# Kernel optimization log

Hardware: AMD Instinct MI355X
Metric: run time of the kernel (lower is better)

The kernel has to match this reference:

```python
import jax, jax.numpy as jnp
import numpy as np

T, B, S = 32, 64, 128
V, WV, ENC, DEC, ATT = 50000, 512, 512, 512, 512
LAYERS, POOL = 2, 2
IN0 = WV + ENC  # input_feed concat


def _gru_cell(x, h, W_ih, b_ih, W_hh, b_hh):
    gi = x @ W_ih.T + b_ih
    gh = h @ W_hh.T + b_hh
    i_r, i_z, i_n = jnp.split(gi, 3, axis=-1)
    h_r, h_z, h_n = jnp.split(gh, 3, axis=-1)
    r = jax.nn.sigmoid(i_r + h_r)
    z = jax.nn.sigmoid(i_z + h_z)
    n = jnp.tanh(i_n + r * h_n)
    return (1.0 - z) * n + z * h


def setup_inputs() -> dict:
    key = jax.random.key(0)
    ks = iter(jax.random.split(key, 32))
    d = {}
    d['input'] = jax.random.randint(next(ks), (T, B), 0, V)
    d['hidden'] = jax.random.normal(next(ks), (LAYERS, B, DEC), jnp.float32)
    d['context'] = jax.random.normal(next(ks), (S, B, ENC), jnp.float32)
    d['src_pad_mask'] = jnp.zeros((B, S), jnp.float32)
    d['init_att'] = jax.random.normal(next(ks), (B, ENC), jnp.float32)
    sc = 0.05
    d['emb_W'] = jax.random.normal(next(ks), (V, WV), jnp.float32) * sc
    # stacked GRU params (layer0 input IN0, layer1 input DEC)
    d['W_ih0'] = jax.random.normal(next(ks), (3 * DEC, IN0), jnp.float32) * sc
    d['b_ih0'] = jnp.zeros((3 * DEC,), jnp.float32)
    d['W_hh0'] = jax.random.normal(next(ks), (3 * DEC, DEC), jnp.float32) * sc
    d['b_hh0'] = jnp.zeros((3 * DEC,), jnp.float32)
    d['W_ih1'] = jax.random.normal(next(ks), (3 * DEC, DEC), jnp.float32) * sc
    d['b_ih1'] = jnp.zeros((3 * DEC,), jnp.float32)
    d['W_hh1'] = jax.random.normal(next(ks), (3 * DEC, DEC), jnp.float32) * sc
    d['b_hh1'] = jnp.zeros((3 * DEC,), jnp.float32)
    # concat attention
    d['W_pre'] = jax.random.normal(next(ks), (ATT, ENC), jnp.float32) * sc
    d['b_pre'] = jnp.zeros((ATT,), jnp.float32)
    d['W_q'] = jax.random.normal(next(ks), (ATT, DEC), jnp.float32) * sc
    d['w_v'] = jax.random.normal(next(ks), (ATT,), jnp.float32) * sc
    # copy switch
    d['W_copy'] = jax.random.normal(next(ks), (1, ENC + DEC), jnp.float32) * sc
    d['b_copy'] = jnp.zeros((1,), jnp.float32)
    # readout
    d['W_read'] = jax.random.normal(next(ks), (DEC, WV + DEC + ENC), jnp.float32) * sc
    d['b_read'] = jnp.zeros((DEC,), jnp.float32)
    return d


def reference(input, hidden, context, src_pad_mask, init_att, emb_W,
              W_ih0, b_ih0, W_hh0, b_hh0, W_ih1, b_ih1, W_hh1, b_hh1,
              W_pre, b_pre, W_q, w_v, W_copy, b_copy, W_read, b_read):
    emb = emb_W[input]                     # [T,B,WV]
    ctx_bse = jnp.transpose(context, (1, 0, 2))  # [B,S,ENC]
    precompute = jnp.einsum('bse,ae->bsa', ctx_bse, W_pre) + b_pre  # [B,S,ATT]
    neg_inf = jnp.finfo(jnp.float32).min

    def step(carry, emb_t):
        h, cur_ctx = carry
        x = jnp.concatenate([emb_t, cur_ctx], axis=1)  # input_feed
        h0 = _gru_cell(x, h[0], W_ih0, b_ih0, W_hh0, b_hh0)
        out = _gru_cell(h0, h[1], W_ih1, b_ih1, W_hh1, b_hh1)
        h_new = jnp.stack([h0, out])
        # concat attention
        q = out @ W_q.T                                  # [B,ATT]
        energy = jnp.tanh(precompute + q[:, None, :]) @ w_v  # [B,S]
        energy = jnp.where(src_pad_mask > 0.5, neg_inf, energy)
        attn = jax.nn.softmax(energy, axis=-1)
        new_ctx = jnp.einsum('bs,bse->be', attn, ctx_bse)
        copy_prob = jax.nn.sigmoid(
            jnp.concatenate([out, new_ctx], axis=1) @ W_copy.T + b_copy)  # [B,1]
        readout = jnp.concatenate([emb_t, out, new_ctx], axis=1) @ W_read.T + b_read
        maxout = jnp.max(readout.reshape(B, DEC // POOL, POOL), axis=-1)  # [B,DEC/POOL]
        return (h_new, new_ctx), (maxout, attn, copy_prob)

    (hidden_f, cur_ctx_f), (g_outputs, c_outputs, copy_gates) = jax.lax.scan(
        step, (hidden, init_att), emb)
    attn_last = c_outputs[-1]
    return g_outputs, c_outputs, copy_gates, hidden_f, attn_last, cur_ctx_f
```

## Files before the change

kernel.cpp:

```cpp
#include <hip/hip_runtime.h>


#define OFF_EGI    0
#define OFF_EREAD  3145728
#define OFF_ATTPRE 4194304
#define OFF_Q      8388608
#define OFF_GI     8454144
#define OFF_GH     8847360
#define OFF_GI1    8847360
#define OFF_GH1    9240576
#define OFF_RO     9437184
#define OFF_H0     9568256
#define OFF_H1     9633792
#define OFF_CTX    9699328

#define OO_G    0
#define OO_C    524288
#define OO_CP   786432
#define OO_HID  788480
#define OO_AL   854016
#define OO_CTXF 862208

__device__ __forceinline__ float sigm(float x) {
    x = fminf(fmaxf(x, -30.f), 30.f);
    return 1.0f / (1.0f + __expf(-x));
}
__device__ __forceinline__ float tanh_(float x) {
    x = fminf(fmaxf(x, -15.f), 15.f);
    float e = __expf(-2.0f * x);
    return (1.0f - e) / (1.0f + e);
}
__device__ __forceinline__ float gru_out(float ir, float iz, float in_,
                                         float hr, float hz, float hn, float hp) {
    float r = sigm(ir + hr), z = sigm(iz + hz);
    float n = tanh_(in_ + r * hn);
    return (1.f - z) * n + z * hp;
}

__device__ __forceinline__ void gemm64(
    const float* __restrict__ xrow, const float* __restrict__ wrow,
    int kt0, int nkt, float* lds_x, float* lds_w,
    float* __restrict__ outp, int JW, int orow0, int j0,
    const float* __restrict__ addp, int addmode, int addJW)
{
    const int tid = threadIdx.x;
    const int tb4 = tid >> 4, tj4 = tid & 15;
    float acc[4][4];
#pragma unroll
    for (int a = 0; a < 4; ++a)
#pragma unroll
        for (int b = 0; b < 4; ++b) acc[a][b] = 0.f;

    for (int kt = kt0; kt < kt0 + nkt; ++kt) {
        const int kb = kt << 6;
        __syncthreads();
        {
            const int rl = tid >> 2;
#pragma unroll
            for (int i = 0; i < 4; ++i) {
                const int kk = ((tid & 3) << 4) + (i << 2);
                float4 xv = *(const float4*)(xrow + kb + kk);
                float4 wv = *(const float4*)(wrow + kb + kk);
                lds_x[(kk + 0) * 64 + rl] = xv.x;
                lds_x[(kk + 1) * 64 + rl] = xv.y;
                lds_x[(kk + 2) * 64 + rl] = xv.z;
                lds_x[(kk + 3) * 64 + rl] = xv.w;
                lds_w[(kk + 0) * 64 + rl] = wv.x;
                lds_w[(kk + 1) * 64 + rl] = wv.y;
                lds_w[(kk + 2) * 64 + rl] = wv.z;
                lds_w[(kk + 3) * 64 + rl] = wv.w;
            }
        }
        __syncthreads();
#pragma unroll 4
        for (int kk = 0; kk < 64; ++kk) {
            float4 xv = *(const float4*)(lds_x + kk * 64 + tb4 * 4);
            float4 wv = *(const float4*)(lds_w + kk * 64 + tj4 * 4);
            acc[0][0] += xv.x * wv.x; acc[0][1] += xv.x * wv.y;
            acc[0][2] += xv.x * wv.z; acc[0][3] += xv.x * wv.w;
            acc[1][0] += xv.y * wv.x; acc[1][1] += xv.y * wv.y;
            acc[1][2] += xv.y * wv.z; acc[1][3] += xv.y * wv.w;
            acc[2][0] += xv.z * wv.x; acc[2][1] += xv.z * wv.y;
            acc[2][2] += xv.z * wv.z; acc[2][3] += xv.z * wv.w;
            acc[3][0] += xv.w * wv.x; acc[3][1] += xv.w * wv.y;
            acc[3][2] += xv.w * wv.z; acc[3][3] += xv.w * wv.w;
        }
    }
#pragma unroll
    for (int ib = 0; ib < 4; ++ib) {
        const int row = tb4 * 4 + ib;
        const int jc = j0 + tj4 * 4;
        float4 r;
        r.x = acc[ib][0]; r.y = acc[ib][1]; r.z = acc[ib][2]; r.w = acc[ib][3];
        if (addmode == 1) {
            float4 bv = *(const float4*)(addp + jc);
            r.x += bv.x; r.y += bv.y; r.z += bv.z; r.w += bv.w;
        } else if (addmode == 2) {
            float4 bv = *(const float4*)(addp + (size_t)(orow0 + row) * addJW + jc);
            r.x += bv.x; r.y += bv.y; r.z += bv.z; r.w += bv.w;
        }
        *(float4*)(outp + (size_t)(orow0 + row) * JW + jc) = r;
    }
}

__global__ __launch_bounds__(256)
void k_upfront(const int* __restrict__ inp, const float* __restrict__ hid,
               const float* __restrict__ ctxin, const float* __restrict__ init_att,
               const float* __restrict__ embW,
               const float* __restrict__ W_ih0, const float* __restrict__ b_ih0,
               const float* __restrict__ W_read, const float* __restrict__ b_read,
               const float* __restrict__ W_pre, const float* __restrict__ b_pre,
               float* __restrict__ wsf)
{
    __shared__ float lds_x[4096], lds_w[4096];
    const int jid = blockIdx.x, tid = threadIdx.x, rl = tid >> 2;
    if (jid < 768) {
        const int mt = jid / 24, jt = jid % 24, j0 = jt << 6;
        const int idx = inp[mt * 64 + rl];
        gemm64(embW + (size_t)idx * 512, W_ih0 + (size_t)(j0 + rl) * 1024,
               0, 8, lds_x, lds_w, wsf + OFF_EGI, 1536, mt << 6, j0, b_ih0, 1, 0);
    } else if (jid < 1024) {
        const int r = jid - 768, mt = r >> 3, jt = r & 7, j0 = jt << 6;
        const int idx = inp[mt * 64 + rl];
        gemm64(embW + (size_t)idx * 512, W_read + (size_t)(j0 + rl) * 1536,
               0, 8, lds_x, lds_w, wsf + OFF_EREAD, 512, mt << 6, j0, b_read, 1, 0);
    } else if (jid < 2048) {
        const int r = jid - 1024, mt = r >> 3, jt = r & 7, j0 = jt << 6;
        const int m = (mt << 6) + rl, b = m >> 7, s = m & 127;
        gemm64(ctxin + (size_t)((s << 6) + b) * 512, W_pre + (size_t)(j0 + rl) * 512,
               0, 8, lds_x, lds_w, wsf + OFF_ATTPRE, 512, mt << 6, j0, b_pre, 1, 0);
    } else {
        const int job = jid - 2048, buf = job >> 1, half = job & 1;
        const float* src = buf == 0 ? hid : (buf == 1 ? hid + 32768 : init_att);
        float* dst = wsf + (buf == 0 ? OFF_H0 : (buf == 1 ? OFF_H1 : OFF_CTX)) + 32768;
        for (int i = 0; i < 64; ++i) {
            int e = half * 16384 + i * 256 + tid;
            dst[e] = src[e];
        }
    }
}

__global__ __launch_bounds__(256)
void k_gates(int t, const float* __restrict__ W_ih0,
             const float* __restrict__ W_hh0, const float* __restrict__ b_hh0,
             const float* __restrict__ W_hh1, const float* __restrict__ b_hh1,
             const float* __restrict__ W_read, float* __restrict__ wsf)
{
    __shared__ float lds_x[4096], lds_w[4096];
    const int blk = blockIdx.x, tid = threadIdx.x, rl = tid >> 2;
    const int prv = (t & 1) ^ 1;
    const float* ctx_prv = wsf + OFF_CTX + prv * 32768;
    const float* h0_prv  = wsf + OFF_H0 + prv * 32768;
    const float* h1_prv  = wsf + OFF_H1 + prv * 32768;
    if (blk < 96) {
        const int jt = blk >> 2, kq = blk & 3, j0 = jt << 6;
        gemm64(ctx_prv + rl * 512, W_ih0 + (size_t)(j0 + rl) * 1024 + 512,
               kq * 2, 2, lds_x, lds_w, wsf + OFF_GI + kq * 98304, 1536, 0, j0,
               wsf + OFF_EGI + (size_t)t * 98304, kq == 0 ? 2 : 0, 1536);
    } else if (blk < 192) {
        const int r = blk - 96, jt = r >> 2, kq = r & 3, j0 = jt << 6;
        gemm64(h0_prv + rl * 512, W_hh0 + (size_t)(j0 + rl) * 512,
               kq * 2, 2, lds_x, lds_w, wsf + OFF_GH + kq * 98304, 1536, 0, j0,
               b_hh0, kq == 0 ? 1 : 0, 0);
    } else if (blk < 240) {
        const int r = blk - 192, jt = r >> 1, kh = r & 1, j0 = jt << 6;
        gemm64(h1_prv + rl * 512, W_hh1 + (size_t)(j0 + rl) * 512,
               kh * 4, 4, lds_x, lds_w, wsf + OFF_GH1 + kh * 98304, 1536, 0, j0,
               b_hh1, kh == 0 ? 1 : 0, 0);
    } else {
        if (t == 0) return;
        const int r = blk - 240, mat = r >> 4, kh = (r >> 3) & 1, jt = r & 7, j0 = jt << 6;
        const float* X = mat ? ctx_prv : h1_prv;
        gemm64(X + rl * 512, W_read + (size_t)(j0 + rl) * 1536 + 512 + mat * 512,
               kh * 4, 4, lds_x, lds_w, wsf + OFF_RO + (mat * 2 + kh) * 32768, 512, 0, j0,
               nullptr, 0, 0);
    }
}

__global__ __launch_bounds__(256)
void k_h0(int t, float* __restrict__ wsf, float* __restrict__ dout)
{
    const int blk = blockIdx.x, tid = threadIdx.x;
    const int cur = t & 1, prv = cur ^ 1;
    if (blk < 16) {
        float* h0_cur = wsf + OFF_H0 + cur * 32768;
        const float* h0_prv = wsf + OFF_H0 + prv * 32768;
        const float* GIp = wsf + OFF_GI;
        const float* GHp = wsf + OFF_GH;
#pragma unroll
        for (int i = 0; i < 8; ++i) {
            const int e = (blk << 11) + (i << 8) + tid;
            const int b = e >> 9, c = e & 511;
            const int base = b * 1536 + c;
            float gr = 0, gz = 0, gn = 0, hr = 0, hz = 0, hn = 0;
#pragma unroll
            for (int p = 0; p < 4; ++p) {
                gr += GIp[p * 98304 + base];
                gz += GIp[p * 98304 + base + 512];
                gn += GIp[p * 98304 + base + 1024];
                hr += GHp[p * 98304 + base];
                hz += GHp[p * 98304 + base + 512];
                hn += GHp[p * 98304 + base + 1024];
            }
            float rr = sigm(gr + hr), zz = sigm(gz + hz);
            float nn = tanh_(gn + rr * hn);
            h0_cur[b * 512 + c] = (1.f - zz) * nn + zz * h0_prv[b * 512 + c];
        }
    } else {
        if (t == 0) return;
        const int r = blk - 16;
        const float* ERp = wsf + OFF_EREAD + (size_t)(t - 1) * 32768;
        const float* ROp = wsf + OFF_RO;
#pragma unroll
        for (int i = 0; i < 8; ++i) {
            const int e = (r << 11) + (i << 8) + tid;
            const int b = e >> 8, j2 = e & 255;
            const int bi = b * 512 + (j2 << 1);
            float v0 = ERp[bi] + ROp[bi] + ROp[32768 + bi] + ROp[65536 + bi] + ROp[98304 + bi];
            float v1 = ERp[bi + 1] + ROp[bi + 1] + ROp[32768 + bi + 1] + ROp[65536 + bi + 1] + ROp[98304 + bi + 1];
            dout[OO_G + (size_t)(t - 1) * 16384 + b * 256 + j2] = fmaxf(v0, v1);
        }
    }
}

__global__ __launch_bounds__(256)
void k_gi1(int t, const float* __restrict__ W_ih1, const float* __restrict__ b_ih1,
           float* __restrict__ wsf)
{
    __shared__ float lds_x[4096], lds_w[4096];
    const int blk = blockIdx.x, tid = threadIdx.x, rl = tid >> 2;
    const int cur = t & 1;
    const float* h0_cur = wsf + OFF_H0 + cur * 32768;
    const int jt = blk >> 2, kq = blk & 3, j0 = jt << 6;
    gemm64(h0_cur + rl * 512, W_ih1 + (size_t)(j0 + rl) * 512,
           kq * 2, 2, lds_x, lds_w, wsf + OFF_GI1 + kq * 98304, 1536, 0, j0,
           b_ih1, kq == 0 ? 1 : 0, 0);
}

__global__ __launch_bounds__(256)
void k_oq(int t, const float* __restrict__ W_q, float* __restrict__ wsf)
{
    __shared__ float s_o[64 * 129];
    __shared__ float s_w[64 * 64];
    const int blk = blockIdx.x, tid = threadIdx.x;
    const int cur = t & 1, prv = cur ^ 1;
    const float* GI1p = wsf + OFF_GI1;
    const float* GH1p = wsf + OFF_GH1;
    const float* h1_prv = wsf + OFF_H1 + prv * 32768;
    float* h1_cur = wsf + OFF_H1 + cur * 32768;
    const int jt = blk >> 2, kq = blk & 3, j0 = jt << 6;
    const int kbase = kq << 7;
    const int tb4 = tid >> 4, tj4 = tid & 15, rl = tid >> 2;

#pragma unroll
    for (int i = 0; i < 8; ++i) {
        const int f = (i << 8) + tid;
        const int b = f >> 5, c4 = f & 31;
        const int c = kbase + (c4 << 2);
        float4 ir = {0,0,0,0}, iz = ir, in4 = ir, hr = ir, hz = ir, hn = ir;
#pragma unroll
        for (int p = 0; p < 4; ++p) {
            const float* gp = GI1p + p * 98304 + b * 1536 + c;
            float4 a0 = *(const float4*)(gp);
            float4 a1 = *(const float4*)(gp + 512);
            float4 a2 = *(const float4*)(gp + 1024);
            ir.x += a0.x; ir.y += a0.y; ir.z += a0.z; ir.w += a0.w;
            iz.x += a1.x; iz.y += a1.y; iz.z += a1.z; iz.w += a1.w;
            in4.x += a2.x; in4.y += a2.y; in4.z += a2.z; in4.w += a2.w;
        }
#pragma unroll
        for (int p = 0; p < 2; ++p) {
            const float* gp = GH1p + p * 98304 + b * 1536 + c;
            float4 a0 = *(const float4*)(gp);
            float4 a1 = *(const float4*)(gp + 512);
            float4 a2 = *(const float4*)(gp + 1024);
            hr.x += a0.x; hr.y += a0.y; hr.z += a0.z; hr.w += a0.w;
            hz.x += a1.x; hz.y += a1.y; hz.z += a1.z; hz.w += a1.w;
            hn.x += a2.x; hn.y += a2.y; hn.z += a2.z; hn.w += a2.w;
        }
        float4 hp = *(const float4*)(h1_prv + b * 512 + c);
        float4 o;
        o.x = gru_out(ir.x, iz.x, in4.x, hr.x, hz.x, hn.x, hp.x);
        o.y = gru_out(ir.y, iz.y, in4.y, hr.y, hz.y, hn.y, hp.y);
        o.z = gru_out(ir.z, iz.z, in4.z, hr.z, hz.z, hn.z, hp.z);
        o.w = gru_out(ir.w, iz.w, in4.w, hr.w, hz.w, hn.w, hp.w);
        const int kl = c4 << 2;
        s_o[b * 129 + kl + 0] = o.x;
        s_o[b * 129 + kl + 1] = o.y;
        s_o[b * 129 + kl + 2] = o.z;
        s_o[b * 129 + kl + 3] = o.w;
        if (jt == 0) *(float4*)(h1_cur + b * 512 + c) = o;
    }

    float acc[4][4];
#pragma unroll
    for (int a = 0; a < 4; ++a)
#pragma unroll
        for (int b = 0; b < 4; ++b) acc[a][b] = 0.f;

    for (int kt = 0; kt < 2; ++kt) {
        __syncthreads();
        {
            const float* wrow = W_q + (size_t)(j0 + rl) * 512 + kbase + kt * 64;
#pragma unroll
            for (int i = 0; i < 4; ++i) {
                const int kk = ((tid & 3) << 4) + (i << 2);
                float4 wv = *(const float4*)(wrow + kk);
                s_w[(kk + 0) * 64 + rl] = wv.x;
                s_w[(kk + 1) * 64 + rl] = wv.y;
                s_w[(kk + 2) * 64 + rl] = wv.z;
                s_w[(kk + 3) * 64 + rl] = wv.w;
            }
        }
        __syncthreads();
#pragma unroll 4
        for (int kk = 0; kk < 64; ++kk) {
            const int ka = kt * 64 + kk;
            float x0 = s_o[(tb4 * 4 + 0) * 129 + ka];
            float x1 = s_o[(tb4 * 4 + 1) * 129 + ka];
            float x2 = s_o[(tb4 * 4 + 2) * 129 + ka];
            float x3 = s_o[(tb4 * 4 + 3) * 129 + ka];
            float4 wv = *(const float4*)(s_w + kk * 64 + tj4 * 4);
            acc[0][0] += x0 * wv.x; acc[0][1] += x0 * wv.y; acc[0][2] += x0 * wv.z; acc[0][3] += x0 * wv.w;
            acc[1][0] += x1 * wv.x; acc[1][1] += x1 * wv.y; acc[1][2] += x1 * wv.z; acc[1][3] += x1 * wv.w;
            acc[2][0] += x2 * wv.x; acc[2][1] += x2 * wv.y; acc[2][2] += x2 * wv.z; acc[2][3] += x2 * wv.w;
            acc[3][0] += x3 * wv.x; acc[3][1] += x3 * wv.y; acc[3][2] += x3 * wv.z; acc[3][3] += x3 * wv.w;
        }
    }
    float* Qp = wsf + OFF_Q + kq * 32768;
#pragma unroll
    for (int ib = 0; ib < 4; ++ib) {
        float4 r;
        r.x = acc[ib][0]; r.y = acc[ib][1]; r.z = acc[ib][2]; r.w = acc[ib][3];
        *(float4*)(Qp + (size_t)(tb4 * 4 + ib) * 512 + j0 + tj4 * 4) = r;
    }
}

__global__ __launch_bounds__(256)
void k_att(int t, const float* __restrict__ ctxin, const float* __restrict__ maskp,
           const float* __restrict__ w_v, const float* __restrict__ W_copy,
           const float* __restrict__ b_copy, float* __restrict__ wsf,
           float* __restrict__ dout)
{
    __shared__ float s_q[512];
    __shared__ float s_e[128];
    __shared__ float s_at[128];
    __shared__ float s_ctx[512];
    __shared__ float s_red[256];
    const int b = blockIdx.x, tid = threadIdx.x;
    const int cur = t & 1;
    float* ctx_cur = wsf + OFF_CTX + cur * 32768;
    const float* h1_cur = wsf + OFF_H1 + cur * 32768;
    const float* Qp = wsf + OFF_Q;
#pragma unroll
    for (int h = 0; h < 2; ++h) {
        const int a = h * 256 + tid;
        s_q[a] = Qp[b * 512 + a] + Qp[32768 + b * 512 + a]
               + Qp[65536 + b * 512 + a] + Qp[98304 + b * 512 + a];
    }
    __syncthreads();
    {
        const int wid = tid >> 6, lane = tid & 63;
        for (int s = wid; s < 128; s += 4) {
            const float* pre = wsf + OFF_ATTPRE + ((size_t)b * 128 + s) * 512;
            float acc = 0.f;
#pragma unroll
            for (int i = 0; i < 8; ++i) {
                const int a = lane + (i << 6);
                acc += tanh_(pre[a] + s_q[a]) * w_v[a];
            }
#pragma unroll
            for (int d2 = 1; d2 < 64; d2 <<= 1) acc += __shfl_xor(acc, d2, 64);
            if (lane == 0)
                s_e[s] = (maskp[b * 128 + s] > 0.5f) ? -3.0e38f : acc;
        }
    }
    __syncthreads();
    if (tid < 64) {
        float e0 = s_e[tid], e1 = s_e[tid + 64];
        float mx = fmaxf(e0, e1);
#pragma unroll
        for (int d2 = 1; d2 < 64; d2 <<= 1) mx = fmaxf(mx, __shfl_xor(mx, d2, 64));
        float x0 = __expf(e0 - mx), x1 = __expf(e1 - mx);
        float sm = x0 + x1;
#pragma unroll
        for (int d2 = 1; d2 < 64; d2 <<= 1) sm += __shfl_xor(sm, d2, 64);
        float inv = 1.f / sm;
        x0 *= inv; x1 *= inv;
        s_at[tid] = x0; s_at[tid + 64] = x1;
        float* co = dout + OO_C + ((size_t)t * 64 + b) * 128;
        co[tid] = x0; co[tid + 64] = x1;
        if (t == 31) {
            dout[OO_AL + b * 128 + tid] = x0;
            dout[OO_AL + b * 128 + tid + 64] = x1;
        }
    }
    __syncthreads();
    for (int e = tid; e < 512; e += 256) {
        float acc = 0.f;
        for (int s = 0; s < 128; ++s)
            acc = fmaf(s_at[s], ctxin[((size_t)s * 64 + b) * 512 + e], acc);
        s_ctx[e] = acc;
        ctx_cur[b * 512 + e] = acc;
    }
    __syncthreads();
    {
        float part = 0.f;
        for (int i2 = tid; i2 < 512; i2 += 256)
            part += h1_cur[b * 512 + i2] * W_copy[i2] + s_ctx[i2] * W_copy[512 + i2];
        s_red[tid] = part;
        __syncthreads();
        for (int d2 = 128; d2 > 0; d2 >>= 1) {
            if (tid < d2) s_red[tid] += s_red[tid + d2];
            __syncthreads();
        }
        if (tid == 0)
            dout[OO_CP + t * 64 + b] = sigm(s_red[0] + b_copy[0]);
    }
}

__global__ __launch_bounds__(256)
void k_epi1(const float* __restrict__ W_read, float* __restrict__ wsf,
            float* __restrict__ dout)
{
    __shared__ float lds_x[4096], lds_w[4096];
    const int blk = blockIdx.x, tid = threadIdx.x, rl = tid >> 2;
    if (blk < 32) {
        const int mat = blk >> 4, kh = (blk >> 3) & 1, jt = blk & 7, j0 = jt << 6;
        const float* X = mat ? (wsf + OFF_CTX + 32768) : (wsf + OFF_H1 + 32768);
        gemm64(X + rl * 512, W_read + (size_t)(j0 + rl) * 1536 + 512 + mat * 512,
               kh * 4, 4, lds_x, lds_w, wsf + OFF_RO + (mat * 2 + kh) * 32768, 512, 0, j0,
               nullptr, 0, 0);
    } else if (blk < 34) {
        const int base = (blk - 32) * 16384;
        for (int i = 0; i < 64; ++i) { int e = base + i * 256 + tid; dout[OO_HID + e] = wsf[OFF_H0 + 32768 + e]; }
    } else if (blk < 36) {
        const int base = (blk - 34) * 16384;
        for (int i = 0; i < 64; ++i) { int e = base + i * 256 + tid; dout[OO_HID + 32768 + e] = wsf[OFF_H1 + 32768 + e]; }
    } else {
        const int base = (blk - 36) * 16384;
        for (int i = 0; i < 64; ++i) { int e = base + i * 256 + tid; dout[OO_CTXF + e] = wsf[OFF_CTX + 32768 + e]; }
    }
}

__global__ __launch_bounds__(256)
void k_epi2(float* __restrict__ wsf, float* __restrict__ dout)
{
    const int blk = blockIdx.x, tid = threadIdx.x;
    const float* ERp = wsf + OFF_EREAD + (size_t)31 * 32768;
    const float* ROp = wsf + OFF_RO;
#pragma unroll
    for (int i = 0; i < 8; ++i) {
        const int e = (blk << 11) + (i << 8) + tid;
        const int b = e >> 8, j2 = e & 255;
        const int bi = b * 512 + (j2 << 1);
        float v0 = ERp[bi] + ROp[bi] + ROp[32768 + bi] + ROp[65536 + bi] + ROp[98304 + bi];
        float v1 = ERp[bi + 1] + ROp[bi + 1] + ROp[32768 + bi + 1] + ROp[65536 + bi + 1] + ROp[98304 + bi + 1];
        dout[OO_G + (size_t)31 * 16384 + b * 256 + j2] = fmaxf(v0, v1);
    }
}

extern "C" void kernel_launch(void* const* d_in, const int* in_sizes, int n_in,
                              void* d_out, int out_size, void* d_ws, size_t ws_size,
                              hipStream_t stream) {
    const int*   inp      = (const int*)d_in[0];
    const float* hid      = (const float*)d_in[1];
    const float* ctxin    = (const float*)d_in[2];
    const float* maskp    = (const float*)d_in[3];
    const float* init_att = (const float*)d_in[4];
    const float* embW     = (const float*)d_in[5];
    const float* W_ih0    = (const float*)d_in[6];
    const float* b_ih0    = (const float*)d_in[7];
    const float* W_hh0    = (const float*)d_in[8];
    const float* b_hh0    = (const float*)d_in[9];
    const float* W_ih1    = (const float*)d_in[10];
    const float* b_ih1    = (const float*)d_in[11];
    const float* W_hh1    = (const float*)d_in[12];
    const float* b_hh1    = (const float*)d_in[13];
    const float* W_pre    = (const float*)d_in[14];
    const float* b_pre    = (const float*)d_in[15];
    const float* W_q      = (const float*)d_in[16];
    const float* w_v      = (const float*)d_in[17];
    const float* W_copy   = (const float*)d_in[18];
    const float* b_copy   = (const float*)d_in[19];
    const float* W_read   = (const float*)d_in[20];
    const float* b_read   = (const float*)d_in[21];
    float* dout = (float*)d_out;
    float* wsf  = (float*)d_ws;

    k_upfront<<<dim3(2054), dim3(256), 0, stream>>>(
        inp, hid, ctxin, init_att, embW, W_ih0, b_ih0, W_read, b_read, W_pre, b_pre, wsf);

    for (int t = 0; t < 32; ++t) {
        k_gates<<<dim3(272), dim3(256), 0, stream>>>(t, W_ih0, W_hh0, b_hh0, W_hh1, b_hh1, W_read, wsf);
        k_h0<<<dim3(24), dim3(256), 0, stream>>>(t, wsf, dout);
        k_gi1<<<dim3(96), dim3(256), 0, stream>>>(t, W_ih1, b_ih1, wsf);
        k_oq<<<dim3(32), dim3(256), 0, stream>>>(t, W_q, wsf);
        k_att<<<dim3(64), dim3(256), 0, stream>>>(t, ctxin, maskp, w_v, W_copy, b_copy, wsf, dout);
    }
    k_epi1<<<dim3(38), dim3(256), 0, stream>>>(W_read, wsf, dout);
    k_epi2<<<dim3(8), dim3(256), 0, stream>>>(wsf, dout);
}
```

Before: 3.134 ms.

## Use bf16 MFMA for recurrent GEMMs and fuse GRU layer-1 and query into attention

Converts the recurrent weights, the transposed context and the hidden states to bf16 once up front. The per-step GEMMs then run on 16x16x32 bf16 MFMA instructions with a swizzled LDS stage, and the split-K partial buffers are removed. The layer-1 GRU update and the W_q projection are fused into the attention kernel, which also reads a bf16 [b,s,e] copy of the context. This cuts launches per step from 5 to 4 and reduces memory traffic. The trade-off is bf16 rounding in the recurrence and dropped clamps in sigmoid and tanh.

After: 3.349 ms. +6.8%, slower.

```diff
diff --git a/kernel.cpp b/kernel.cpp
--- a/kernel.cpp
+++ b/kernel.cpp
@@ -1,18 +1,33 @@
 #include <hip/hip_runtime.h>
 
+
+typedef unsigned short u16;
+using bf16x8 = __attribute__((ext_vector_type(8))) short;
+using f32x4  = __attribute__((ext_vector_type(4))) float;
 
 #define OFF_EGI    0
 #define OFF_EREAD  3145728
 #define OFF_ATTPRE 4194304
-#define OFF_Q      8388608
-#define OFF_GI     8454144
-#define OFF_GH     8847360
-#define OFF_GI1    8847360
-#define OFF_GH1    9240576
-#define OFF_RO     9437184
-#define OFF_H0     9568256
-#define OFF_H1     9633792
-#define OFF_CTX    9699328
+#define OFF_GI0    8388608
+#define OFF_GH0    8486912
+#define OFF_GH1    8585216
+#define OFF_GI1    8683520
+#define OFF_RO0    8781824
+#define OFF_RO1    8814592
+#define OFF_H0     8847360
+#define OFF_H1     8912896
+#define OFF_CTX    8978432
+
+#define UB_WIH0C   18087936
+#define UB_WHH0    18874368
+#define UB_WHH1    19660800
+#define UB_WIH1    20447232
+#define UB_WRO     21233664
+#define UB_WRC     21495808
+#define UB_CTXT    21757952
+#define UB_H0B     25952256
+#define UB_H1B     25985024
+#define UB_CTXB    26017792
 
 #define OO_G    0
 #define OO_C    524288
@@ -22,11 +37,10 @@
 #define OO_CTXF 862208
 
 __device__ __forceinline__ float sigm(float x) {
-    x = fminf(fmaxf(x, -30.f), 30.f);
     return 1.0f / (1.0f + __expf(-x));
 }
 __device__ __forceinline__ float tanh_(float x) {
-    x = fminf(fmaxf(x, -15.f), 15.f);
+    x = fmaxf(x, -15.f);
     float e = __expf(-2.0f * x);
     return (1.0f - e) / (1.0f + e);
 }
@@ -35,6 +49,13 @@
     float r = sigm(ir + hr), z = sigm(iz + hz);
     float n = tanh_(in_ + r * hn);
     return (1.f - z) * n + z * hp;
+}
+__device__ __forceinline__ u16 f2b(float x) {
+    unsigned u = __float_as_uint(x);
+    return (u16)((u + 0x7FFFu + ((u >> 16) & 1u)) >> 16);
+}
+__device__ __forceinline__ float b2f(unsigned u) {
+    return __uint_as_float(u << 16);
 }
 
 __device__ __forceinline__ void gemm64(
@@ -103,16 +124,71 @@
     }
 }
 
+__device__ __forceinline__ void stage_bf16(const u16* __restrict__ Xg, u16* sX) {
+    const int tid = threadIdx.x;
+#pragma unroll
+    for (int p = 0; p < 16; ++p) {
+        const int chunk = p * 256 + tid;
+        const int row = chunk >> 6, cb16 = chunk & 63;
+        const int src = row * 1024 + cb16 * 16;
+        const int dst = row * 1024 + ((cb16 * 16) ^ ((row & 7) << 4));
+        *(float4*)((char*)sX + dst) = *(const float4*)((const char*)Xg + src);
+    }
+}
+
+__device__ __forceinline__ void mfma_gemm64(const u16* sX, const u16* __restrict__ Wg,
+        float* __restrict__ outp, int JW,
+        const float* __restrict__ addp, int mode, int addJW)
+{
+    const int tid = threadIdx.x;
+    const int w = tid >> 6, l = tid & 63;
+    const int l15 = l & 15, lhi = l >> 4;
+    f32x4 acc0 = {0.f,0.f,0.f,0.f}, acc1 = acc0, acc2 = acc0, acc3 = acc0;
+    const int arow = w * 16 + l15;
+    const char* aptr = (const char*)sX;
+    const int abase = arow * 1024 + lhi * 16;
+    const int aswz = (arow & 7) << 4;
+#pragma unroll 4
+    for (int ks = 0; ks < 16; ++ks) {
+        bf16x8 a = *(const bf16x8*)(aptr + ((abase + ks * 64) ^ aswz));
+        const u16* wp = Wg + l15 * 512 + ks * 32 + lhi * 8;
+        bf16x8 b0 = *(const bf16x8*)(wp);
+        bf16x8 b1 = *(const bf16x8*)(wp + 16 * 512);
+        bf16x8 b2 = *(const bf16x8*)(wp + 32 * 512);
+        bf16x8 b3 = *(const bf16x8*)(wp + 48 * 512);
+        acc0 = __builtin_amdgcn_mfma_f32_16x16x32_bf16(a, b0, acc0, 0, 0, 0);
+        acc1 = __builtin_amdgcn_mfma_f32_16x16x32_bf16(a, b1, acc1, 0, 0, 0);
+        acc2 = __builtin_amdgcn_mfma_f32_16x16x32_bf16(a, b2, acc2, 0, 0, 0);
+        acc3 = __builtin_amdgcn_mfma_f32_16x16x32_bf16(a, b3, acc3, 0, 0, 0);
+    }
+    f32x4 accs[4] = {acc0, acc1, acc2, acc3};
+#pragma unroll
+    for (int cb = 0; cb < 4; ++cb) {
+        const int col = cb * 16 + l15;
+#pragma unroll
+        for (int r = 0; r < 4; ++r) {
+            const int row = w * 16 + lhi * 4 + r;
+            float v = accs[cb][r];
+            if (mode == 1) v += addp[col];
+            else if (mode == 2) v += addp[row * addJW + col];
+            outp[(size_t)row * JW + col] = v;
+        }
+    }
+}
+
 __global__ __launch_bounds__(256)
 void k_upfront(const int* __restrict__ inp, const float* __restrict__ hid,
                const float* __restrict__ ctxin, const float* __restrict__ init_att,
                const float* __restrict__ embW,
                const float* __restrict__ W_ih0, const float* __restrict__ b_ih0,
+               const float* __restrict__ W_hh0, const float* __restrict__ W_hh1,
+               const float* __restrict__ W_ih1,
                const float* __restrict__ W_read, const float* __restrict__ b_read,
                const float* __restrict__ W_pre, const float* __restrict__ b_pre,
                float* __restrict__ wsf)
 {
     __shared__ float lds_x[4096], lds_w[4096];
+    u16* wsu = (u16*)wsf;
     const int jid = blockIdx.x, tid = threadIdx.x, rl = tid >> 2;
     if (jid < 768) {
         const int mt = jid / 24, jt = jid % 24, j0 = jt << 6;
@@ -129,7 +205,7 @@
         const int m = (mt << 6) + rl, b = m >> 7, s = m & 127;
         gemm64(ctxin + (size_t)((s << 6) + b) * 512, W_pre + (size_t)(j0 + rl) * 512,
                0, 8, lds_x, lds_w, wsf + OFF_ATTPRE, 512, mt << 6, j0, b_pre, 1, 0);
-    } else {
+    } else if (jid < 2054) {
         const int job = jid - 2048, buf = job >> 1, half = job & 1;
         const float* src = buf == 0 ? hid : (buf == 1 ? hid + 32768 : init_att);
         float* dst = wsf + (buf == 0 ? OFF_H0 : (buf == 1 ? OFF_H1 : OFF_CTX)) + 32768;
@@ -137,228 +213,214 @@
             int e = half * 16384 + i * 256 + tid;
             dst[e] = src[e];
         }
-    }
-}
-
-__global__ __launch_bounds__(256)
-void k_gates(int t, const float* __restrict__ W_ih0,
-             const float* __restrict__ W_hh0, const float* __restrict__ b_hh0,
-             const float* __restrict__ W_hh1, const float* __restrict__ b_hh1,
-             const float* __restrict__ W_read, float* __restrict__ wsf)
-{
-    __shared__ float lds_x[4096], lds_w[4096];
-    const int blk = blockIdx.x, tid = threadIdx.x, rl = tid >> 2;
-    const int prv = (t & 1) ^ 1;
-    const float* ctx_prv = wsf + OFF_CTX + prv * 32768;
-    const float* h0_prv  = wsf + OFF_H0 + prv * 32768;
-    const float* h1_prv  = wsf + OFF_H1 + prv * 32768;
-    if (blk < 96) {
-        const int jt = blk >> 2, kq = blk & 3, j0 = jt << 6;
-        gemm64(ctx_prv + rl * 512, W_ih0 + (size_t)(j0 + rl) * 1024 + 512,
-               kq * 2, 2, lds_x, lds_w, wsf + OFF_GI + kq * 98304, 1536, 0, j0,
-               wsf + OFF_EGI + (size_t)t * 98304, kq == 0 ? 2 : 0, 1536);
-    } else if (blk < 192) {
-        const int r = blk - 96, jt = r >> 2, kq = r & 3, j0 = jt << 6;
-        gemm64(h0_prv + rl * 512, W_hh0 + (size_t)(j0 + rl) * 512,
-               kq * 2, 2, lds_x, lds_w, wsf + OFF_GH + kq * 98304, 1536, 0, j0,
-               b_hh0, kq == 0 ? 1 : 0, 0);
-    } else if (blk < 240) {
-        const int r = blk - 192, jt = r >> 1, kh = r & 1, j0 = jt << 6;
-        gemm64(h1_prv + rl * 512, W_hh1 + (size_t)(j0 + rl) * 512,
-               kh * 4, 4, lds_x, lds_w, wsf + OFF_GH1 + kh * 98304, 1536, 0, j0,
-               b_hh1, kh == 0 ? 1 : 0, 0);
+    } else if (jid < 2278) {
+        const int w = jid - 2054;
+        if (w < 48) {
+            for (int i = 0; i < 64; ++i) {
+                int e = w * 16384 + i * 256 + tid;
+                int j = e >> 9, k = e & 511;
+                wsu[UB_WIH0C + e] = f2b(W_ih0[(size_t)j * 1024 + 512 + k]);
+            }
+        } else if (w < 96) {
+            for (int i = 0; i < 64; ++i) {
+                int e = (w - 48) * 16384 + i * 256 + tid;
+                wsu[UB_WHH0 + e] = f2b(W_hh0[e]);
+            }
+        } else if (w < 144) {
+            for (int i = 0; i < 64; ++i) {
+                int e = (w - 96) * 16384 + i * 256 + tid;
+                wsu[UB_WHH1 + e] = f2b(W_hh1[e]);
+            }
+        } else if (w < 192) {
+            for (int i = 0; i < 64; ++i) {
+                int e = (w - 144) * 16384 + i * 256 + tid;
+                wsu[UB_WIH1 + e] = f2b(W_ih1[e]);
+            }
+        } else if (w < 208) {
+            for (int i = 0; i < 64; ++i) {
+                int e = (w - 192) * 16384 + i * 256 + tid;
+                int j = e >> 9, k = e & 511;
+                wsu[UB_WRO + e] = f2b(W_read[(size_t)j * 1536 + 512 + k]);
+            }
+        } else {
+            for (int i = 0; i < 64; ++i) {
+                int e = (w - 208) * 16384 + i * 256 + tid;
+                int j = e >> 9, k = e & 511;
+                wsu[UB_WRC + e] = f2b(W_read[(size_t)j * 1536 + 1024 + k]);
+            }
+        }
+    } else if (jid < 2534) {
+        const int w2 = jid - 2278;
+        for (int rr = 0; rr < 32; ++rr) {
+            const int r = w2 * 32 + rr;
+            const int b = r >> 7, s = r & 127;
+            const float* src = ctxin + ((size_t)s * 64 + b) * 512;
+#pragma unroll
+            for (int h = 0; h < 2; ++h) {
+                int e = h * 256 + tid;
+                wsu[UB_CTXT + (size_t)r * 512 + e] = f2b(src[e]);
+            }
+        }
+    } else {
+        const int job = jid - 2534;
+        const float* src = job == 0 ? hid : (job == 1 ? hid + 32768 : init_att);
+        u16* dst = wsu + (job == 0 ? UB_H0B : (job == 1 ? UB_H1B : UB_CTXB));
+        for (int i = 0; i < 128; ++i) {
+            int e = i * 256 + tid;
+            dst[e] = f2b(src[e]);
+        }
+    }
+}
+
+__global__ __launch_bounds__(256)
+void k_pA(int t, const float* __restrict__ b_hh0, const float* __restrict__ b_hh1,
+          float* __restrict__ wsf)
+{
+    __shared__ u16 sX[64 * 512];
+    u16* wsu = (u16*)wsf;
+    const int blk = blockIdx.x;
+    if (blk < 24) {
+        stage_bf16(wsu + UB_CTXB, sX);
+        __syncthreads();
+        const int jt = blk, j0 = jt << 6;
+        mfma_gemm64(sX, wsu + UB_WIH0C + jt * 32768, wsf + OFF_GI0 + j0, 1536,
+                    wsf + OFF_EGI + (size_t)t * 98304 + j0, 2, 1536);
+    } else if (blk < 48) {
+        stage_bf16(wsu + UB_H0B, sX);
+        __syncthreads();
+        const int jt = blk - 24, j0 = jt << 6;
+        mfma_gemm64(sX, wsu + UB_WHH0 + jt * 32768, wsf + OFF_GH0 + j0, 1536,
+                    b_hh0 + j0, 1, 0);
+    } else if (blk < 72) {
+        stage_bf16(wsu + UB_H1B, sX);
+        __syncthreads();
+        const int jt = blk - 48, j0 = jt << 6;
+        mfma_gemm64(sX, wsu + UB_WHH1 + jt * 32768, wsf + OFF_GH1 + j0, 1536,
+                    b_hh1 + j0, 1, 0);
+    } else if (blk < 80) {
+        if (t == 0) return;
+        stage_bf16(wsu + UB_H1B, sX);
+        __syncthreads();
+        const int jt = blk - 72, j0 = jt << 6;
+        mfma_gemm64(sX, wsu + UB_WRO + jt * 32768, wsf + OFF_RO0 + j0, 512,
+                    nullptr, 0, 0);
     } else {
         if (t == 0) return;
-        const int r = blk - 240, mat = r >> 4, kh = (r >> 3) & 1, jt = r & 7, j0 = jt << 6;
-        const float* X = mat ? ctx_prv : h1_prv;
-        gemm64(X + rl * 512, W_read + (size_t)(j0 + rl) * 1536 + 512 + mat * 512,
-               kh * 4, 4, lds_x, lds_w, wsf + OFF_RO + (mat * 2 + kh) * 32768, 512, 0, j0,
-               nullptr, 0, 0);
-    }
-}
-
-__global__ __launch_bounds__(256)
-void k_h0(int t, float* __restrict__ wsf, float* __restrict__ dout)
-{
+        stage_bf16(wsu + UB_CTXB, sX);
+        __syncthreads();
+        const int jt = blk - 80, j0 = jt << 6;
+        mfma_gemm64(sX, wsu + UB_WRC + jt * 32768, wsf + OFF_RO1 + j0, 512,
+                    nullptr, 0, 0);
+    }
+}
+
+__global__ __launch_bounds__(256)
+void k_pB(int t, float* __restrict__ wsf, float* __restrict__ dout)
+{
+    u16* wsu = (u16*)wsf;
     const int blk = blockIdx.x, tid = threadIdx.x;
     const int cur = t & 1, prv = cur ^ 1;
     if (blk < 16) {
         float* h0_cur = wsf + OFF_H0 + cur * 32768;
         const float* h0_prv = wsf + OFF_H0 + prv * 32768;
-        const float* GIp = wsf + OFF_GI;
-        const float* GHp = wsf + OFF_GH;
+        const float* GIp = wsf + OFF_GI0;
+        const float* GHp = wsf + OFF_GH0;
+        u16* h0b = wsu + UB_H0B;
 #pragma unroll
         for (int i = 0; i < 8; ++i) {
             const int e = (blk << 11) + (i << 8) + tid;
             const int b = e >> 9, c = e & 511;
             const int base = b * 1536 + c;
-            float gr = 0, gz = 0, gn = 0, hr = 0, hz = 0, hn = 0;
-#pragma unroll
-            for (int p = 0; p < 4; ++p) {
-                gr += GIp[p * 98304 + base];
-                gz += GIp[p * 98304 + base + 512];
-                gn += GIp[p * 98304 + base + 1024];
-                hr += GHp[p * 98304 + base];
-                hz += GHp[p * 98304 + base + 512];
-                hn += GHp[p * 98304 + base + 1024];
-            }
-            float rr = sigm(gr + hr), zz = sigm(gz + hz);
-            float nn = tanh_(gn + rr * hn);
-            h0_cur[b * 512 + c] = (1.f - zz) * nn + zz * h0_prv[b * 512 + c];
+            float v = gru_out(GIp[base], GIp[base + 512], GIp[base + 1024],
+                              GHp[base], GHp[base + 512], GHp[base + 1024],
+                              h0_prv[b * 512 + c]);
+            h0_cur[b * 512 + c] = v;
+            h0b[b * 512 + c] = f2b(v);
         }
     } else {
         if (t == 0) return;
         const int r = blk - 16;
         const float* ERp = wsf + OFF_EREAD + (size_t)(t - 1) * 32768;
-        const float* ROp = wsf + OFF_RO;
+        const float* R0 = wsf + OFF_RO0;
+        const float* R1 = wsf + OFF_RO1;
 #pragma unroll
         for (int i = 0; i < 8; ++i) {
             const int e = (r << 11) + (i << 8) + tid;
             const int b = e >> 8, j2 = e & 255;
             const int bi = b * 512 + (j2 << 1);
-            float v0 = ERp[bi] + ROp[bi] + ROp[32768 + bi] + ROp[65536 + bi] + ROp[98304 + bi];
-            float v1 = ERp[bi + 1] + ROp[bi + 1] + ROp[32768 + bi + 1] + ROp[65536 + bi + 1] + ROp[98304 + bi + 1];
+            float v0 = ERp[bi]     + R0[bi]     + R1[bi];
+            float v1 = ERp[bi + 1] + R0[bi + 1] + R1[bi + 1];
             dout[OO_G + (size_t)(t - 1) * 16384 + b * 256 + j2] = fmaxf(v0, v1);
         }
     }
 }
 
 __global__ __launch_bounds__(256)
-void k_gi1(int t, const float* __restrict__ W_ih1, const float* __restrict__ b_ih1,
-           float* __restrict__ wsf)
-{
-    __shared__ float lds_x[4096], lds_w[4096];
-    const int blk = blockIdx.x, tid = threadIdx.x, rl = tid >> 2;
-    const int cur = t & 1;
-    const float* h0_cur = wsf + OFF_H0 + cur * 32768;
-    const int jt = blk >> 2, kq = blk & 3, j0 = jt << 6;
-    gemm64(h0_cur + rl * 512, W_ih1 + (size_t)(j0 + rl) * 512,
-           kq * 2, 2, lds_x, lds_w, wsf + OFF_GI1 + kq * 98304, 1536, 0, j0,
-           b_ih1, kq == 0 ? 1 : 0, 0);
-}
-
-__global__ __launch_bounds__(256)
-void k_oq(int t, const float* __restrict__ W_q, float* __restrict__ wsf)
-{
-    __shared__ float s_o[64 * 129];
-    __shared__ float s_w[64 * 64];
-    const int blk = blockIdx.x, tid = threadIdx.x;
-    const int cur = t & 1, prv = cur ^ 1;
-    const float* GI1p = wsf + OFF_GI1;
-    const float* GH1p = wsf + OFF_GH1;
-    const float* h1_prv = wsf + OFF_H1 + prv * 32768;
-    float* h1_cur = wsf + OFF_H1 + cur * 32768;
-    const int jt = blk >> 2, kq = blk & 3, j0 = jt << 6;
-    const int kbase = kq << 7;
-    const int tb4 = tid >> 4, tj4 = tid & 15, rl = tid >> 2;
-
-#pragma unroll
-    for (int i = 0; i < 8; ++i) {
-        const int f = (i << 8) + tid;
-        const int b = f >> 5, c4 = f & 31;
-        const int c = kbase + (c4 << 2);
-        float4 ir = {0,0,0,0}, iz = ir, in4 = ir, hr = ir, hz = ir, hn = ir;
-#pragma unroll
-        for (int p = 0; p < 4; ++p) {
-            const float* gp = GI1p + p * 98304 + b * 1536 + c;
-            float4 a0 = *(const float4*)(gp);
-            float4 a1 = *(const float4*)(gp + 512);
-            float4 a2 = *(const float4*)(gp + 1024);
-            ir.x += a0.x; ir.y += a0.y; ir.z += a0.z; ir.w += a0.w;
-            iz.x += a1.x; iz.y += a1.y; iz.z += a1.z; iz.w += a1.w;
-            in4.x += a2.x; in4.y += a2.y; in4.z += a2.z; in4.w += a2.w;
-        }
-#pragma unroll
-        for (int p = 0; p < 2; ++p) {
-            const float* gp = GH1p + p * 98304 + b * 1536 + c;
-            float4 a0 = *(const float4*)(gp);
-            float4 a1 = *(const float4*)(gp + 512);
-            float4 a2 = *(const float4*)(gp + 1024);
-            hr.x += a0.x; hr.y += a0.y; hr.z += a0.z; hr.w += a0.w;
-            hz.x += a1.x; hz.y += a1.y; hz.z += a1.z; hz.w += a1.w;
-            hn.x += a2.x; hn.y += a2.y; hn.z += a2.z; hn.w += a2.w;
-        }
-        float4 hp = *(const float4*)(h1_prv + b * 512 + c);
-        float4 o;
-        o.x = gru_out(ir.x, iz.x, in4.x, hr.x, hz.x, hn.x, hp.x);
-        o.y = gru_out(ir.y, iz.y, in4.y, hr.y, hz.y, hn.y, hp.y);
-        o.z = gru_out(ir.z, iz.z, in4.z, hr.z, hz.z, hn.z, hp.z);
-        o.w = gru_out(ir.w, iz.w, in4.w, hr.w, hz.w, hn.w, hp.w);
-        const int kl = c4 << 2;
-        s_o[b * 129 + kl + 0] = o.x;
-        s_o[b * 129 + kl + 1] = o.y;
-        s_o[b * 129 + kl + 2] = o.z;
-        s_o[b * 129 + kl + 3] = o.w;
-        if (jt == 0) *(float4*)(h1_cur + b * 512 + c) = o;
-    }
-
-    float acc[4][4];
-#pragma unroll
-    for (int a = 0; a < 4; ++a)
-#pragma unroll
-        for (int b = 0; b < 4; ++b) acc[a][b] = 0.f;
-
-    for (int kt = 0; kt < 2; ++kt) {
-        __syncthreads();
-        {
-            const float* wrow = W_q + (size_t)(j0 + rl) * 512 + kbase + kt * 64;
-#pragma unroll
-            for (int i = 0; i < 4; ++i) {
-                const int kk = ((tid & 3) << 4) + (i << 2);
-                float4 wv = *(const float4*)(wrow + kk);
-                s_w[(kk + 0) * 64 + rl] = wv.x;
-                s_w[(kk + 1) * 64 + rl] = wv.y;
-                s_w[(kk + 2) * 64 + rl] = wv.z;
-                s_w[(kk + 3) * 64 + rl] = wv.w;
-            }
-        }
-        __syncthreads();
-#pragma unroll 4
-        for (int kk = 0; kk < 64; ++kk) {
-            const int ka = kt * 64 + kk;
-            float x0 = s_o[(tb4 * 4 + 0) * 129 + ka];
-            float x1 = s_o[(tb4 * 4 + 1) * 129 + ka];
-            float x2 = s_o[(tb4 * 4 + 2) * 129 + ka];
-            float x3 = s_o[(tb4 * 4 + 3) * 129 + ka];
-            float4 wv = *(const float4*)(s_w + kk * 64 + tj4 * 4);
-            acc[0][0] += x0 * wv.x; acc[0][1] += x0 * wv.y; acc[0][2] += x0 * wv.z; acc[0][3] += x0 * wv.w;
-            acc[1][0] += x1 * wv.x; acc[1][1] += x1 * wv.y; acc[1][2] += x1 * wv.z; acc[1][3] += x1 * wv.w;
-            acc[2][0] += x2 * wv.x; acc[2][1] += x2 * wv.y; acc[2][2] += x2 * wv.z; acc[2][3] += x2 * wv.w;
-            acc[3][0] += x3 * wv.x; acc[3][1] += x3 * wv.y; acc[3][2] += x3 * wv.z; acc[3][3] += x3 * wv.w;
-        }
-    }
-    float* Qp = wsf + OFF_Q + kq * 32768;
-#pragma unroll
-    for (int ib = 0; ib < 4; ++ib) {
-        float4 r;
-        r.x = acc[ib][0]; r.y = acc[ib][1]; r.z = acc[ib][2]; r.w = acc[ib][3];
-        *(float4*)(Qp + (size_t)(tb4 * 4 + ib) * 512 + j0 + tj4 * 4) = r;
-    }
-}
-
-__global__ __launch_bounds__(256)
-void k_att(int t, const float* __restrict__ ctxin, const float* __restrict__ maskp,
-           const float* __restrict__ w_v, const float* __restrict__ W_copy,
-           const float* __restrict__ b_copy, float* __restrict__ wsf,
-           float* __restrict__ dout)
-{
+void k_pC(const float* __restrict__ b_ih1, float* __restrict__ wsf)
+{
+    __shared__ u16 sX[64 * 512];
+    u16* wsu = (u16*)wsf;
+    stage_bf16(wsu + UB_H0B, sX);
+    __syncthreads();
+    const int jt = blockIdx.x, j0 = jt << 6;
+    mfma_gemm64(sX, wsu + UB_WIH1 + jt * 32768, wsf + OFF_GI1 + j0, 1536,
+                b_ih1 + j0, 1, 0);
+}
+
+__global__ __launch_bounds__(256)
+void k_pD(int t, const float* __restrict__ maskp, const float* __restrict__ w_v,
+          const float* __restrict__ W_q, const float* __restrict__ W_copy,
+          const float* __restrict__ b_copy, float* __restrict__ wsf,
+          float* __restrict__ dout)
+{
+    __shared__ float s_out[512];
     __shared__ float s_q[512];
     __shared__ float s_e[128];
     __shared__ float s_at[128];
     __shared__ float s_ctx[512];
     __shared__ float s_red[256];
+    u16* wsu = (u16*)wsf;
     const int b = blockIdx.x, tid = threadIdx.x;
-    const int cur = t & 1;
-    float* ctx_cur = wsf + OFF_CTX + cur * 32768;
-    const float* h1_cur = wsf + OFF_H1 + cur * 32768;
-    const float* Qp = wsf + OFF_Q;
-#pragma unroll
-    for (int h = 0; h < 2; ++h) {
-        const int a = h * 256 + tid;
-        s_q[a] = Qp[b * 512 + a] + Qp[32768 + b * 512 + a]
-               + Qp[65536 + b * 512 + a] + Qp[98304 + b * 512 + a];
+    const int cur = t & 1, prv = cur ^ 1;
+
+    {
+        const float* GI1p = wsf + OFF_GI1 + b * 1536;
+        const float* GH1p = wsf + OFF_GH1 + b * 1536;
+        const float* h1p = wsf + OFF_H1 + prv * 32768 + b * 512;
+        float* h1c = wsf + OFF_H1 + cur * 32768 + b * 512;
+        u16* h1b = wsu + UB_H1B + b * 512;
+        const int c0 = tid * 2;
+        float2 gi_r = *(const float2*)(GI1p + c0);
+        float2 gi_z = *(const float2*)(GI1p + 512 + c0);
+        float2 gi_n = *(const float2*)(GI1p + 1024 + c0);
+        float2 gh_r = *(const float2*)(GH1p + c0);
+        float2 gh_z = *(const float2*)(GH1p + 512 + c0);
+        float2 gh_n = *(const float2*)(GH1p + 1024 + c0);
+        float2 hp = *(const float2*)(h1p + c0);
+        float o0 = gru_out(gi_r.x, gi_z.x, gi_n.x, gh_r.x, gh_z.x, gh_n.x, hp.x);
+        float o1 = gru_out(gi_r.y, gi_z.y, gi_n.y, gh_r.y, gh_z.y, gh_n.y, hp.y);
+        s_out[c0] = o0; s_out[c0 + 1] = o1;
+        *(float2*)(h1c + c0) = make_float2(o0, o1);
+        *(unsigned*)(h1b + c0) = (unsigned)f2b(o0) | ((unsigned)f2b(o1) << 16);
     }
     __syncthreads();
+
+    {
+        float q0 = 0.f, q1 = 0.f;
+        const float* w0 = W_q + (size_t)tid * 512;
+        const float* w1 = W_q + (size_t)(tid + 256) * 512;
+#pragma unroll 8
+        for (int c = 0; c < 512; c += 4) {
+            float4 ov = *(const float4*)(s_out + c);
+            float4 a0 = *(const float4*)(w0 + c);
+            float4 a1 = *(const float4*)(w1 + c);
+            q0 += ov.x * a0.x + ov.y * a0.y + ov.z * a0.z + ov.w * a0.w;
+            q1 += ov.x * a1.x + ov.y * a1.y + ov.z * a1.z + ov.w * a1.w;
+        }
+        s_q[tid] = q0; s_q[tid + 256] = q1;
+    }
+    __syncthreads();
+
     {
         const int wid = tid >> 6, lane = tid & 63;
         for (int s = wid; s < 128; s += 4) {
@@ -376,6 +438,7 @@
         }
     }
     __syncthreads();
+
     if (tid < 64) {
         float e0 = s_e[tid], e1 = s_e[tid + 64];
         float mx = fmaxf(e0, e1);
@@ -396,18 +459,30 @@
         }
     }
     __syncthreads();
-    for (int e = tid; e < 512; e += 256) {
-        float acc = 0.f;
-        for (int s = 0; s < 128; ++s)
-            acc = fmaf(s_at[s], ctxin[((size_t)s * 64 + b) * 512 + e], acc);
-        s_ctx[e] = acc;
-        ctx_cur[b * 512 + e] = acc;
+
+    {
+        const int e0 = tid * 2;
+        const u16* ct = wsu + UB_CTXT + (size_t)b * 65536 + e0;
+        float a0 = 0.f, a1 = 0.f;
+#pragma unroll 4
+        for (int s = 0; s < 128; ++s) {
+            float at = s_at[s];
+            unsigned pv = *(const unsigned*)(ct + s * 512);
+            a0 = fmaf(at, b2f(pv & 0xffffu), a0);
+            a1 = fmaf(at, b2f(pv >> 16), a1);
+        }
+        s_ctx[e0] = a0; s_ctx[e0 + 1] = a1;
+        float* cc = wsf + OFF_CTX + cur * 32768 + b * 512;
+        *(float2*)(cc + e0) = make_float2(a0, a1);
+        *(unsigned*)(wsu + UB_CTXB + b * 512 + e0) =
+            (unsigned)f2b(a0) | ((unsigned)f2b(a1) << 16);
     }
     __syncthreads();
+
     {
         float part = 0.f;
         for (int i2 = tid; i2 < 512; i2 += 256)
-            part += h1_cur[b * 512 + i2] * W_copy[i2] + s_ctx[i2] * W_copy[512 + i2];
+            part += s_out[i2] * W_copy[i2] + s_ctx[i2] * W_copy[512 + i2];
         s_red[tid] = part;
         __syncthreads();
         for (int d2 = 128; d2 > 0; d2 >>= 1) {
@@ -420,42 +495,48 @@
 }
 
 __global__ __launch_bounds__(256)
-void k_epi1(const float* __restrict__ W_read, float* __restrict__ wsf,
-            float* __restrict__ dout)
-{
-    __shared__ float lds_x[4096], lds_w[4096];
-    const int blk = blockIdx.x, tid = threadIdx.x, rl = tid >> 2;
-    if (blk < 32) {
-        const int mat = blk >> 4, kh = (blk >> 3) & 1, jt = blk & 7, j0 = jt << 6;
-        const float* X = mat ? (wsf + OFF_CTX + 32768) : (wsf + OFF_H1 + 32768);
-        gemm64(X + rl * 512, W_read + (size_t)(j0 + rl) * 1536 + 512 + mat * 512,
-               kh * 4, 4, lds_x, lds_w, wsf + OFF_RO + (mat * 2 + kh) * 32768, 512, 0, j0,
-               nullptr, 0, 0);
-    } else if (blk < 34) {
-        const int base = (blk - 32) * 16384;
-        for (int i = 0; i < 64; ++i) { int e = base + i * 256 + tid; dout[OO_HID + e] = wsf[OFF_H0 + 32768 + e]; }
-    } else if (blk < 36) {
-        const int base = (blk - 34) * 16384;
-        for (int i = 0; i < 64; ++i) { int e = base + i * 256 + tid; dout[OO_HID + 32768 + e] = wsf[OFF_H1 + 32768 + e]; }
+void k_roF(float* __restrict__ wsf, float* __restrict__ dout)
+{
+    __shared__ u16 sX[64 * 512];
+    u16* wsu = (u16*)wsf;
+    const int blk = blockIdx.x, tid = threadIdx.x;
+    if (blk < 8) {
+        stage_bf16(wsu + UB_H1B, sX);
+        __syncthreads();
+        const int j0 = blk << 6;
+        mfma_gemm64(sX, wsu + UB_WRO + blk * 32768, wsf + OFF_RO0 + j0, 512,
+                    nullptr, 0, 0);
+    } else if (blk < 16) {
+        stage_bf16(wsu + UB_CTXB, sX);
+        __syncthreads();
+        const int jt = blk - 8, j0 = jt << 6;
+        mfma_gemm64(sX, wsu + UB_WRC + jt * 32768, wsf + OFF_RO1 + j0, 512,
+                    nullptr, 0, 0);
     } else {
-        const int base = (blk - 36) * 16384;
-        for (int i = 0; i < 64; ++i) { int e = base + i * 256 + tid; dout[OO_CTXF + e] = wsf[OFF_CTX + 32768 + e]; }
-    }
-}
-
-__global__ __launch_bounds__(256)
-void k_epi2(float* __restrict__ wsf, float* __restrict__ dout)
+        const int job = blk - 16, buf = job >> 1, half = job & 1;
+        const float* src = wsf + (buf == 0 ? OFF_H0 : (buf == 1 ? OFF_H1 : OFF_CTX)) + 32768;
+        float* dst = dout + (buf == 0 ? OO_HID : (buf == 1 ? OO_HID + 32768 : OO_CTXF));
+        for (int i = 0; i < 64; ++i) {
+            int e = half * 16384 + i * 256 + tid;
+            dst[e] = src[e];
+        }
+    }
+}
+
+__global__ __launch_bounds__(256)
+void k_fin(float* __restrict__ wsf, float* __restrict__ dout)
 {
     const int blk = blockIdx.x, tid = threadIdx.x;
     const float* ERp = wsf + OFF_EREAD + (size_t)31 * 32768;
-    const float* ROp = wsf + OFF_RO;
+    const float* R0 = wsf + OFF_RO0;
+    const float* R1 = wsf + OFF_RO1;
 #pragma unroll
     for (int i = 0; i < 8; ++i) {
         const int e = (blk << 11) + (i << 8) + tid;
         const int b = e >> 8, j2 = e & 255;
         const int bi = b * 512 + (j2 << 1);
-        float v0 = ERp[bi] + ROp[bi] + ROp[32768 + bi] + ROp[65536 + bi] + ROp[98304 + bi];
-        float v1 = ERp[bi + 1] + ROp[bi + 1] + ROp[32768 + bi + 1] + ROp[65536 + bi + 1] + ROp[98304 + bi + 1];
+        float v0 = ERp[bi]     + R0[bi]     + R1[bi];
+        float v1 = ERp[bi + 1] + R0[bi + 1] + R1[bi + 1];
         dout[OO_G + (size_t)31 * 16384 + b * 256 + j2] = fmaxf(v0, v1);
     }
 }
@@ -488,16 +569,17 @@
     float* dout = (float*)d_out;
     float* wsf  = (float*)d_ws;
 
-    k_upfront<<<dim3(2054), dim3(256), 0, stream>>>(
-        inp, hid, ctxin, init_att, embW, W_ih0, b_ih0, W_read, b_read, W_pre, b_pre, wsf);
+    k_upfront<<<dim3(2537), dim3(256), 0, stream>>>(
+        inp, hid, ctxin, init_att, embW, W_ih0, b_ih0, W_hh0, W_hh1, W_ih1,
+        W_read, b_read, W_pre, b_pre, wsf);
 
     for (int t = 0; t < 32; ++t) {
-        k_gates<<<dim3(272), dim3(256), 0, stream>>>(t, W_ih0, W_hh0, b_hh0, W_hh1, b_hh1, W_read, wsf);
-        k_h0<<<dim3(24), dim3(256), 0, stream>>>(t, wsf, dout);
-        k_gi1<<<dim3(96), dim3(256), 0, stream>>>(t, W_ih1, b_ih1, wsf);
-        k_oq<<<dim3(32), dim3(256), 0, stream>>>(t, W_q, wsf);
-        k_att<<<dim3(64), dim3(256), 0, stream>>>(t, ctxin, maskp, w_v, W_copy, b_copy, wsf, dout);
-    }
-    k_epi1<<<dim3(38), dim3(256), 0, stream>>>(W_read, wsf, dout);
-    k_epi2<<<dim3(8), dim3(256), 0, stream>>>(wsf, dout);
-}
+        k_pA<<<dim3(88), dim3(256), 0, stream>>>(t, b_hh0, b_hh1, wsf);
+        k_pB<<<dim3(24), dim3(256), 0, stream>>>(t, wsf, dout);
+        k_pC<<<dim3(24), dim3(256), 0, stream>>>(b_ih1, wsf);
+        k_pD<<<dim3(64), dim3(256), 0, stream>>>(t, maskp, w_v, W_q, W_copy,
+                                                 b_copy, wsf, dout);
+    }
+    k_roF<<<dim3(22), dim3(256), 0, stream>>>(wsf, dout);
+    k_fin<<<dim3(8), dim3(256), 0, stream>>>(wsf, dout);
+}
```
